# Kernel tuning notes

Hardware: AMD Instinct MI355X
Metric: run time of the kernel (lower is better)

The kernel has to match this reference:

```python
import jax, jax.numpy as jnp
import numpy as np

N_COMP = 16  # sedenion components

def _cd_table(n):
    """Cayley-Dickson basis multiplication table: e_i * e_j = sign[i,j] * e_{idx[i,j]}."""
    if n == 1:
        return np.array([[1]], dtype=np.int64), np.array([[0]], dtype=np.int64)
    m = n // 2
    s, k = _cd_table(m)
    conj = np.where(np.arange(m) == 0, 1, -1)  # conj(e_0)=e_0, conj(e_i)=-e_i
    S = np.zeros((n, n), dtype=np.int64)
    K = np.zeros((n, n), dtype=np.int64)
    for i in range(n):
        for j in range(n):
            if i < m and j < m:          # (a,0)(c,0) = (ac, 0)
                S[i, j] = s[i, j]; K[i, j] = k[i, j]
            elif i < m:                  # (a,0)(0,d) = (0, d a)
                q = j - m
                S[i, j] = s[q, i]; K[i, j] = m + k[q, i]
            elif j < m:                  # (0,b)(c,0) = (0, b c*)
                p = i - m
                S[i, j] = s[p, j] * conj[j]; K[i, j] = m + k[p, j]
            else:                        # (0,b)(0,d) = (-d* b, 0)
                p, q = i - m, j - m
                S[i, j] = -conj[q] * s[q, p]; K[i, j] = k[q, p]
    return S, K

SIGN, IDX = _cd_table(N_COMP)

def _sedenion_kernel(w_comp):
    """Assemble the (16n, 16n) real matrix of the sedenion linear map from 16 (n,n) component weights."""
    blocks = [[None] * N_COMP for _ in range(N_COMP)]
    for i in range(N_COMP):
        for j in range(N_COMP):
            blocks[j][int(IDX[i, j])] = float(SIGN[i, j]) * w_comp[i]
    return jnp.concatenate([jnp.concatenate(row, axis=1) for row in blocks], axis=0)


def setup_inputs() -> dict:
    key = jax.random.key(0)
    k1, k2, k3, k4 = jax.random.split(key, 4)
    B, C, H, W = 8, 96, 256, 256
    x = jax.random.normal(k1, (B, C, H, W), jnp.float32)
    w_comp = jax.random.normal(k2, (N_COMP, C, C), jnp.float32) * 0.02
    proj_w = jax.random.normal(k3, (C, C), jnp.float32) * 0.02
    proj_b = jax.random.normal(k4, (C,), jnp.float32) * 0.02
    return {"x": x, "w_comp": w_comp, "proj_w": proj_w, "proj_b": proj_b}


def reference(x, w_comp, proj_w, proj_b):
    B, C, H, W = x.shape
    h, w = H // 4, W // 4
    # get_window: 'b c (h s1) (w s2) -> b h w (s1 s2 c)' with s1=s2=4
    xw = x.reshape(B, C, h, 4, w, 4).transpose(0, 2, 4, 3, 5, 1).reshape(B, h, w, 16 * C)
    big = _sedenion_kernel(w_comp)          # (16C, 16C)
    y = xw @ big                            # sedenion linear on windowed features
    # reverse_window + 'b c h w -> b h w c' fused: (B,h,w,16C) -> (B,H,W,C)
    y = y.reshape(B, h, w, 4, 4, C).transpose(0, 1, 3, 2, 4, 5).reshape(B, H, W, C)
    y = jax.nn.gelu(y, approximate=False)   # nn.GELU (exact); dropouts are identity (p=0)
    y = y @ proj_w.T + proj_b               # nn.Linear(dim, dim)
    return y.transpose(0, 3, 1, 2)          # 'b h w c -> b c h w'
```

## Files before the change

### kernel.cpp

```cpp
#include <hip/hip_runtime.h>
#include <hip/hip_bf16.h>

typedef __attribute__((ext_vector_type(8))) short short8v;
typedef __attribute__((ext_vector_type(4))) float float4v;

struct SedTab { signed char sgn[256]; signed char idx[256]; };

__device__ inline unsigned short f2bf(float f) {
    __hip_bfloat16 h = __float2bfloat16(f);
    return *reinterpret_cast<unsigned short*>(&h);
}

#define GLOAD_LDS16(g, l) __builtin_amdgcn_global_load_lds( \
    (const __attribute__((address_space(1))) void*)(g), \
    (__attribute__((address_space(3))) void*)(l), 16, 0, 0)

#define VMCNT(n) asm volatile("s_waitcnt vmcnt(" #n ")" ::: "memory")

__global__ __launch_bounds__(256) void build_bigT(
    const float* __restrict__ w_comp, unsigned short* __restrict__ bigT, SedTab tab)
{
    int e = blockIdx.x * 256 + threadIdx.x;
    if (e >= 1536 * 1536) return;
    int n = e / 1536, k = e - n * 1536;
    int t_out = n / 96, c = n - t_out * 96;
    int t_in = k / 96, m = k - t_in * 96;
    int i = tab.idx[t_in * 16 + t_out];
    float s = (float)tab.sgn[t_in * 16 + t_out];
    float v = s * w_comp[(i * 96 + m) * 96 + c];
    bigT[e] = f2bf(v);
}

__global__ __launch_bounds__(256) void window_cast(
    const float* __restrict__ x, unsigned short* __restrict__ xw)
{
    __shared__ unsigned short lds[96][260];
    int blk = blockIdx.x;
    int s1 = blk & 3, hh = (blk >> 2) & 63, b = blk >> 8;
    const float* src = x + (size_t)b * 6291456 + (size_t)(4 * hh + s1) * 256;

    for (int i = threadIdx.x; i < 6144; i += 256) {
        int m = i >> 6;
        int q = (i & 63) << 2;
        float4 v = *(const float4*)(src + (size_t)m * 65536 + q);
        lds[m][q + 0] = f2bf(v.x);
        lds[m][q + 1] = f2bf(v.y);
        lds[m][q + 2] = f2bf(v.z);
        lds[m][q + 3] = f2bf(v.w);
    }
    __syncthreads();
    size_t rowbase = (size_t)((b * 64 + hh) * 64) * 1536 + (size_t)s1 * 384;
    for (int i = threadIdx.x; i < 3072; i += 256) {
        int ww = i / 48, g = i - ww * 48;
        int s2 = g / 12, mg = (g - s2 * 12) * 8;
        int qq = 4 * ww + s2;
        short8v pk;
        #pragma unroll
        for (int j = 0; j < 8; ++j) pk[j] = (short)lds[mg + j][qq];
        *(short8v*)(xw + rowbase + (size_t)ww * 1536 + s2 * 96 + mg) = pk;
    }
}

__global__ __launch_bounds__(512, 2) void gemm_fused(
    const unsigned short* __restrict__ A,
    const unsigned short* __restrict__ Bt,
    const float* __restrict__ pw, const float* __restrict__ pb,
    float* __restrict__ out)
{
    __shared__ __attribute__((aligned(16))) char smem[147456];
    const int t = threadIdx.x;
    const int lane = t & 63, w = t >> 6;
    const int wm = w >> 2, wn = w & 3;
    const int lr = lane & 15, lg = lane >> 4;

    const int bid = blockIdx.x;
    const int wg = (bid & 7) * 128 + (bid >> 3);
    const int nt = wg >> 8, mt = wg & 255;
    const int m0 = mt * 128, n0 = nt * 384;

    float4v acc[4][6];
    #pragma unroll
    for (int i = 0; i < 4; ++i)
        #pragma unroll
        for (int j = 0; j < 6; ++j) acc[i][j] = (float4v)0.0f;

    const int rA = t >> 3;
    const int kc = ((t & 7) ^ (rA & 7)) << 3;
    const unsigned short* gA = A  + (size_t)(m0 + rA) * 1536 + kc;
    const unsigned short* gB = Bt + (size_t)(n0 + rA) * 1536 + kc;
    const int dst = t * 16;

    auto stageA = [&](char* s, int ko) {
        GLOAD_LDS16(gA + ko,             s + dst);
        GLOAD_LDS16(gA + ko + 64 * 1536, s + dst + 8192);
    };
    auto stageB = [&](char* s, int ko) {
        #pragma unroll
        for (int i = 0; i < 6; ++i)
            GLOAD_LDS16(gB + ko + (size_t)i * 64 * 1536, s + dst + i * 8192);
    };

    char* a_rd = smem;          char* a_md = smem + 16384; char* a_wr = smem + 32768;
    char* b_rd = smem + 49152;  char* b_wr = smem + 98304;

    stageA(a_rd, 0); stageB(b_rd, 0); stageA(a_md, 64);
    VMCNT(2);
    __builtin_amdgcn_s_barrier();

    const int c0 = (lg * 8) ^ ((lr & 7) << 3);
    const int c1 = (32 + lg * 8) ^ ((lr & 7) << 3);
    const int ar = wm * 64 + lr;
    const int br = wn * 96 + lr;

    short8v aE[4], aO[4], b0[3], b1[3], b2[3], b3[3];
    {
        const unsigned short* as = (const unsigned short*)a_rd;
        const unsigned short* bs = (const unsigned short*)b_rd;
        #pragma unroll
        for (int mf = 0; mf < 4; ++mf) aE[mf] = *(const short8v*)(as + (ar + mf * 16) * 64 + c0);
        #pragma unroll
        for (int j = 0; j < 3; ++j)    b0[j]  = *(const short8v*)(bs + (br + j * 16) * 64 + c0);
        __builtin_amdgcn_sched_barrier(0);
    }

    int koB = 64, koA = 128;
    for (int kt = 0; kt < 24; ++kt) {
        const unsigned short* as = (const unsigned short*)a_rd;
        const unsigned short* bs = (const unsigned short*)b_rd;

        if (kt < 23) stageB(b_wr, koB);
        __builtin_amdgcn_s_barrier();
        #pragma unroll
        for (int j = 0; j < 3; ++j) b1[j] = *(const short8v*)(bs + (br + (3 + j) * 16) * 64 + c0);
        __builtin_amdgcn_sched_barrier(0);
        __builtin_amdgcn_s_setprio(1);
        #pragma unroll
        for (int mf = 0; mf < 4; ++mf)
            #pragma unroll
            for (int nf = 0; nf < 3; ++nf)
                acc[mf][nf] = __builtin_amdgcn_mfma_f32_16x16x32_bf16(
                    aE[mf], b0[nf], acc[mf][nf], 0, 0, 0);
        __builtin_amdgcn_s_setprio(0);

        __builtin_amdgcn_s_barrier();
        #pragma unroll
        for (int mf = 0; mf < 4; ++mf) aO[mf] = *(const short8v*)(as + (ar + mf * 16) * 64 + c1);
        #pragma unroll
        for (int j = 0; j < 3; ++j)    b2[j]  = *(const short8v*)(bs + (br + j * 16) * 64 + c1);
        __builtin_amdgcn_sched_barrier(0);
        __builtin_amdgcn_s_setprio(1);
        #pragma unroll
        for (int mf = 0; mf < 4; ++mf)
            #pragma unroll
            for (int nf = 0; nf < 3; ++nf)
                acc[mf][3 + nf] = __builtin_amdgcn_mfma_f32_16x16x32_bf16(
                    aE[mf], b1[nf], acc[mf][3 + nf], 0, 0, 0);
        __builtin_amdgcn_s_setprio(0);

        if (kt < 22) stageA(a_wr, koA);
        __builtin_amdgcn_s_barrier();
        #pragma unroll
        for (int j = 0; j < 3; ++j) b3[j] = *(const short8v*)(bs + (br + (3 + j) * 16) * 64 + c1);
        __builtin_amdgcn_sched_barrier(0);
        __builtin_amdgcn_s_setprio(1);
        #pragma unroll
        for (int mf = 0; mf < 4; ++mf)
            #pragma unroll
            for (int nf = 0; nf < 3; ++nf)
                acc[mf][nf] = __builtin_amdgcn_mfma_f32_16x16x32_bf16(
                    aO[mf], b2[nf], acc[mf][nf], 0, 0, 0);
        __builtin_amdgcn_s_setprio(0);

        if (kt < 22)       { VMCNT(2); }
        else if (kt == 22) { VMCNT(0); }
        __builtin_amdgcn_s_barrier();
        if (kt < 23) {
            const unsigned short* asn = (const unsigned short*)a_md;
            const unsigned short* bsn = (const unsigned short*)b_wr;
            #pragma unroll
            for (int mf = 0; mf < 4; ++mf) aE[mf] = *(const short8v*)(asn + (ar + mf * 16) * 64 + c0);
            #pragma unroll
            for (int j = 0; j < 3; ++j)    b0[j]  = *(const short8v*)(bsn + (br + j * 16) * 64 + c0);
        }
        __builtin_amdgcn_sched_barrier(0);
        __builtin_amdgcn_s_setprio(1);
        #pragma unroll
        for (int mf = 0; mf < 4; ++mf)
            #pragma unroll
            for (int nf = 0; nf < 3; ++nf)
                acc[mf][3 + nf] = __builtin_amdgcn_mfma_f32_16x16x32_bf16(
                    aO[mf], b3[nf], acc[mf][3 + nf], 0, 0, 0);
        __builtin_amdgcn_s_setprio(0);

        char* tmp = a_rd; a_rd = a_md; a_md = a_wr; a_wr = tmp;
        tmp = b_rd; b_rd = b_wr; b_wr = tmp;
        koB += 64; koA += 64;
    }

    __syncthreads();

    unsigned short* yl  = (unsigned short*)smem;
    unsigned short* pwl = (unsigned short*)(smem + 106496);
    float*          pbl = (float*)(smem + 126464);

    for (int i = t; i < 9216; i += 512) {
        int r = i / 96, c = i - r * 96;
        pwl[r * 104 + c] = f2bf(pw[i]);
    }
    if (t < 96) pbl[t] = pb[t];

    #pragma unroll
    for (int mf = 0; mf < 4; ++mf) {
        #pragma unroll
        for (int r = 0; r < 4; ++r) {
            const int ww = mf * 16 + lg * 4 + r;
            const int pos = wm * 256 + 4 * ww + wn;
            #pragma unroll
            for (int nf = 0; nf < 6; ++nf) {
                float v = acc[mf][nf][r];
                float g = 0.5f * v * (1.0f + erff(v * 0.70710678118654752f));
                yl[pos * 104 + nf * 16 + lr] = f2bf(g);
            }
        }
    }
    __syncthreads();

    float4v pacc[6][4];
    #pragma unroll
    for (int i = 0; i < 6; ++i)
        #pragma unroll
        for (int j = 0; j < 4; ++j) pacc[i][j] = (float4v)0.0f;

    const int posr = w * 64 + lr;
    #pragma unroll
    for (int ks = 0; ks < 3; ++ks) {
        const int ck = ks * 32 + lg * 8;
        short8v pf[6], yf[4];
        #pragma unroll
        for (int mf2 = 0; mf2 < 6; ++mf2)
            pf[mf2] = *(const short8v*)(pwl + (mf2 * 16 + lr) * 104 + ck);
        #pragma unroll
        for (int nf2 = 0; nf2 < 4; ++nf2)
            yf[nf2] = *(const short8v*)(yl + (posr + nf2 * 16) * 104 + ck);
        #pragma unroll
        for (int mf2 = 0; mf2 < 6; ++mf2)
            #pragma unroll
            for (int nf2 = 0; nf2 < 4; ++nf2)
                pacc[mf2][nf2] = __builtin_amdgcn_mfma_f32_16x16x32_bf16(
                    pf[mf2], yf[nf2], pacc[mf2][nf2], 0, 0, 0);
    }

    const int b  = mt >> 5;
    const int hh = (mt & 31) * 2 + (w >> 2);
    const int p  = 4 * hh + nt;
    const size_t obase = (size_t)b * 6291456 + (size_t)p * 256;
    #pragma unroll
    for (int mf2 = 0; mf2 < 6; ++mf2) {
        #pragma unroll
        for (int r = 0; r < 4; ++r) {
            const int co = mf2 * 16 + lg * 4 + r;
            const float bias = pbl[co];
            #pragma unroll
            for (int nf2 = 0; nf2 < 4; ++nf2) {
                const int q = (w & 3) * 64 + nf2 * 16 + lr;
                out[obase + (size_t)co * 65536 + q] = pacc[mf2][nf2][r] + bias;
            }
        }
    }
}

static void cd_table(int n, int* S, int* K) {
    if (n == 1) { S[0] = 1; K[0] = 0; return; }
    int m = n / 2;
    int s[64], k[64];
    cd_table(m, s, k);
    for (int i = 0; i < n; ++i) {
        for (int j = 0; j < n; ++j) {
            if (i < m && j < m) { S[i*n+j] = s[i*m+j]; K[i*n+j] = k[i*m+j]; }
            else if (i < m) { int q = j - m; S[i*n+j] = s[q*m+i]; K[i*n+j] = m + k[q*m+i]; }
            else if (j < m) { int p = i - m; int cj = (j == 0) ? 1 : -1;
                              S[i*n+j] = s[p*m+j] * cj; K[i*n+j] = m + k[p*m+j]; }
            else { int p = i - m, q = j - m; int cq = (q == 0) ? 1 : -1;
                   S[i*n+j] = -cq * s[q*m+p]; K[i*n+j] = k[q*m+p]; }
        }
    }
}

extern "C" void kernel_launch(void* const* d_in, const int* in_sizes, int n_in,
                              void* d_out, int out_size, void* d_ws, size_t ws_size,
                              hipStream_t stream) {
    const float* x      = (const float*)d_in[0];
    const float* w_comp = (const float*)d_in[1];
    const float* proj_w = (const float*)d_in[2];
    const float* proj_b = (const float*)d_in[3];
    float* out = (float*)d_out;

    unsigned short* Xw   = (unsigned short*)d_ws;
    unsigned short* BigT = (unsigned short*)((char*)d_ws + 100663296);

    int S16[256], K16[256];
    cd_table(16, S16, K16);
    SedTab tab;
    for (int i = 0; i < 16; ++i)
        for (int j = 0; j < 16; ++j) {
            int k = K16[i * 16 + j];
            tab.idx[j * 16 + k] = (signed char)i;
            tab.sgn[j * 16 + k] = (signed char)S16[i * 16 + j];
        }

    hipLaunchKernelGGL(build_bigT, dim3(9216), dim3(256), 0, stream, w_comp, BigT, tab);
    hipLaunchKernelGGL(window_cast, dim3(2048), dim3(256), 0, stream, x, Xw);
    hipLaunchKernelGGL(gemm_fused, dim3(1024), dim3(512), 0, stream,
                       Xw, BigT, proj_w, proj_b, out);
}
```

Before: 302.2 us.

## Restructure GEMM main loop into barrier-fenced phases with split B staging

Reorganizes the K-loop so each of the four MFMA phases starts with its own LDS fragment reads plus a slice of the next B tile's global-to-LDS loads. Phases are fenced by a barrier, an explicit lgkmcnt(0) wait and a closing barrier. The 6 B loads per tile are split into three pairs spread across phases instead of issued at once. The goal is to spread memory traffic evenly and keep waves in lockstep, ping-pong style. The cost is twice as many barriers per iteration and no prefetch of the next iteration's aE/b0 fragments, which could add stalls.

```diff
diff --git a/kernel.cpp b/kernel.cpp
--- a/kernel.cpp
+++ b/kernel.cpp
@@ -16,6 +16,7 @@
     (__attribute__((address_space(3))) void*)(l), 16, 0, 0)
 
 #define VMCNT(n) asm volatile("s_waitcnt vmcnt(" #n ")" ::: "memory")
+#define LGKMCNT0 asm volatile("s_waitcnt lgkmcnt(0)" ::: "memory")
 
 __global__ __launch_bounds__(256) void build_bigT(
     const float* __restrict__ w_comp, unsigned short* __restrict__ bigT, SedTab tab)
@@ -94,16 +95,17 @@
         GLOAD_LDS16(gA + ko,             s + dst);
         GLOAD_LDS16(gA + ko + 64 * 1536, s + dst + 8192);
     };
-    auto stageB = [&](char* s, int ko) {
-        #pragma unroll
-        for (int i = 0; i < 6; ++i)
-            GLOAD_LDS16(gB + ko + (size_t)i * 64 * 1536, s + dst + i * 8192);
+    auto stageB2 = [&](char* s, int ko, int i) {
+        GLOAD_LDS16(gB + ko + (size_t)(2 * i)     * 64 * 1536, s + dst + (2 * i)     * 8192);
+        GLOAD_LDS16(gB + ko + (size_t)(2 * i + 1) * 64 * 1536, s + dst + (2 * i + 1) * 8192);
     };
 
     char* a_rd = smem;          char* a_md = smem + 16384; char* a_wr = smem + 32768;
     char* b_rd = smem + 49152;  char* b_wr = smem + 98304;
 
-    stageA(a_rd, 0); stageB(b_rd, 0); stageA(a_md, 64);
+    stageA(a_rd, 0);
+    stageB2(b_rd, 0, 0); stageB2(b_rd, 0, 1); stageB2(b_rd, 0, 2);
+    stageA(a_md, 64);
     VMCNT(2);
     __builtin_amdgcn_s_barrier();
 
@@ -113,25 +115,20 @@
     const int br = wn * 96 + lr;
 
     short8v aE[4], aO[4], b0[3], b1[3], b2[3], b3[3];
-    {
-        const unsigned short* as = (const unsigned short*)a_rd;
-        const unsigned short* bs = (const unsigned short*)b_rd;
-        #pragma unroll
-        for (int mf = 0; mf < 4; ++mf) aE[mf] = *(const short8v*)(as + (ar + mf * 16) * 64 + c0);
-        #pragma unroll
-        for (int j = 0; j < 3; ++j)    b0[j]  = *(const short8v*)(bs + (br + j * 16) * 64 + c0);
-        __builtin_amdgcn_sched_barrier(0);
-    }
 
     int koB = 64, koA = 128;
     for (int kt = 0; kt < 24; ++kt) {
         const unsigned short* as = (const unsigned short*)a_rd;
         const unsigned short* bs = (const unsigned short*)b_rd;
 
-        if (kt < 23) stageB(b_wr, koB);
-        __builtin_amdgcn_s_barrier();
-        #pragma unroll
-        for (int j = 0; j < 3; ++j) b1[j] = *(const short8v*)(bs + (br + (3 + j) * 16) * 64 + c0);
+        #pragma unroll
+        for (int mf = 0; mf < 4; ++mf) aE[mf] = *(const short8v*)(as + (ar + mf * 16) * 64 + c0);
+        #pragma unroll
+        for (int j = 0; j < 3; ++j)    b0[j]  = *(const short8v*)(bs + (br + j * 16) * 64 + c0);
+        if (kt < 23) stageB2(b_wr, koB, 0);
+        __builtin_amdgcn_sched_barrier(0);
+        __builtin_amdgcn_s_barrier();
+        LGKMCNT0;
         __builtin_amdgcn_sched_barrier(0);
         __builtin_amdgcn_s_setprio(1);
         #pragma unroll
@@ -141,12 +138,14 @@
                 acc[mf][nf] = __builtin_amdgcn_mfma_f32_16x16x32_bf16(
                     aE[mf], b0[nf], acc[mf][nf], 0, 0, 0);
         __builtin_amdgcn_s_setprio(0);
-
-        __builtin_amdgcn_s_barrier();
-        #pragma unroll
-        for (int mf = 0; mf < 4; ++mf) aO[mf] = *(const short8v*)(as + (ar + mf * 16) * 64 + c1);
-        #pragma unroll
-        for (int j = 0; j < 3; ++j)    b2[j]  = *(const short8v*)(bs + (br + j * 16) * 64 + c1);
+        __builtin_amdgcn_s_barrier();
+
+        #pragma unroll
+        for (int j = 0; j < 3; ++j) b1[j] = *(const short8v*)(bs + (br + (3 + j) * 16) * 64 + c0);
+        if (kt < 23) stageB2(b_wr, koB, 1);
+        __builtin_amdgcn_sched_barrier(0);
+        __builtin_amdgcn_s_barrier();
+        LGKMCNT0;
         __builtin_amdgcn_sched_barrier(0);
         __builtin_amdgcn_s_setprio(1);
         #pragma unroll
@@ -156,11 +155,16 @@
                 acc[mf][3 + nf] = __builtin_amdgcn_mfma_f32_16x16x32_bf16(
                     aE[mf], b1[nf], acc[mf][3 + nf], 0, 0, 0);
         __builtin_amdgcn_s_setprio(0);
-
-        if (kt < 22) stageA(a_wr, koA);
-        __builtin_amdgcn_s_barrier();
-        #pragma unroll
-        for (int j = 0; j < 3; ++j) b3[j] = *(const short8v*)(bs + (br + (3 + j) * 16) * 64 + c1);
+        __builtin_amdgcn_s_barrier();
+
+        #pragma unroll
+        for (int mf = 0; mf < 4; ++mf) aO[mf] = *(const short8v*)(as + (ar + mf * 16) * 64 + c1);
+        #pragma unroll
+        for (int j = 0; j < 3; ++j)    b2[j]  = *(const short8v*)(bs + (br + j * 16) * 64 + c1);
+        if (kt < 23) stageB2(b_wr, koB, 2);
+        __builtin_amdgcn_sched_barrier(0);
+        __builtin_amdgcn_s_barrier();
+        LGKMCNT0;
         __builtin_amdgcn_sched_barrier(0);
         __builtin_amdgcn_s_setprio(1);
         #pragma unroll
@@ -170,18 +174,16 @@
                 acc[mf][nf] = __builtin_amdgcn_mfma_f32_16x16x32_bf16(
                     aO[mf], b2[nf], acc[mf][nf], 0, 0, 0);
         __builtin_amdgcn_s_setprio(0);
-
+        __builtin_amdgcn_s_barrier();
+
+        #pragma unroll
+        for (int j = 0; j < 3; ++j) b3[j] = *(const short8v*)(bs + (br + (3 + j) * 16) * 64 + c1);
+        if (kt < 22) stageA(a_wr, koA);
         if (kt < 22)       { VMCNT(2); }
         else if (kt == 22) { VMCNT(0); }
-        __builtin_amdgcn_s_barrier();
-        if (kt < 23) {
-            const unsigned short* asn = (const unsigned short*)a_md;
-            const unsigned short* bsn = (const unsigned short*)b_wr;
-            #pragma unroll
-            for (int mf = 0; mf < 4; ++mf) aE[mf] = *(const short8v*)(asn + (ar + mf * 16) * 64 + c0);
-            #pragma unroll
-            for (int j = 0; j < 3; ++j)    b0[j]  = *(const short8v*)(bsn + (br + j * 16) * 64 + c0);
-        }
+        __builtin_amdgcn_sched_barrier(0);
+        __builtin_amdgcn_s_barrier();
+        LGKMCNT0;
         __builtin_amdgcn_sched_barrier(0);
         __builtin_amdgcn_s_setprio(1);
         #pragma unroll
@@ -191,6 +193,7 @@
                 acc[mf][3 + nf] = __builtin_amdgcn_mfma_f32_16x16x32_bf16(
                     aO[mf], b3[nf], acc[mf][3 + nf], 0, 0, 0);
         __builtin_amdgcn_s_setprio(0);
+        __builtin_amdgcn_s_barrier();
 
         char* tmp = a_rd; a_rd = a_md; a_md = a_wr; a_wr = tmp;
         tmp = b_rd; b_rd = b_wr; b_wr = tmp;
```

After: 306.7 us. About the same (+1.5%).
